# Performance work log

Hardware: AMD Instinct MI355X
Metric: run time of the kernel (lower is better)

## Reference

```python
import jax, jax.numpy as jnp
import numpy as np

N_NODES = 100000
N_EDGES = 800000
N_RADIAL = 16
H_NF = 64
VOCAB = 95  # Embedding(95, h_nf): atomic numbers


def swish(v):
    return v * jax.nn.sigmoid(v)


def setup_inputs() -> dict:
    key = jax.random.key(0)
    ks = jax.random.split(key, 10)
    coords = jax.random.randint(ks[0], (N_NODES,), 0, VOCAB)
    rbf = jax.random.normal(ks[1], (N_EDGES, N_RADIAL), dtype=jnp.float32)
    node_is = jax.random.randint(ks[2], (N_EDGES,), 0, N_NODES)
    node_js = jax.random.randint(ks[3], (N_EDGES,), 0, N_NODES)
    s = 0.05
    emb_W = jax.random.normal(ks[4], (VOCAB, H_NF), dtype=jnp.float32) * s
    W_rbf0 = jax.random.normal(ks[5], (N_RADIAL, H_NF), dtype=jnp.float32) * s
    b_rbf0 = jnp.zeros((H_NF,), dtype=jnp.float32)
    W_lin = jax.random.normal(ks[6], (3 * H_NF, H_NF), dtype=jnp.float32) * s
    b_lin = jnp.zeros((H_NF,), dtype=jnp.float32)
    W_rbf1 = jax.random.normal(ks[7], (N_RADIAL, H_NF), dtype=jnp.float32) * s  # no bias
    return {
        "coords": coords, "rbf": rbf, "node_is": node_is, "node_js": node_js,
        "emb_W": emb_W, "W_rbf0": W_rbf0, "b_rbf0": b_rbf0,
        "W_lin": W_lin, "b_lin": b_lin, "W_rbf1": W_rbf1,
    }


def reference(coords, rbf, node_is, node_js, emb_W, W_rbf0, b_rbf0, W_lin, b_lin, W_rbf1):
    # edge_model of FeatsInitLayer
    x = emb_W[coords]                              # [N, h] gather from embedding table
    rbf0 = swish(rbf @ W_rbf0 + b_rbf0)            # [E, h]
    cat = jnp.concatenate([x[node_is], x[node_js], rbf0], axis=-1)  # [E, 3h]
    e1 = swish(cat @ W_lin + b_lin)                # [E, h]
    e2 = (rbf @ W_rbf1) * e1                       # [E, h]
    return (e1, e2)
```

## Files before the change

### kernel.cpp

```cpp
#include <hip/hip_runtime.h>
#include <stdint.h>


#define N_NODES 100000
#define N_EDGES 800000
#define H_NF 64
#define VOCAB 95
#define NTILES (N_EDGES / 16)

typedef __attribute__((ext_vector_type(8))) short short8;
typedef __attribute__((ext_vector_type(4))) float f32x4;

#define TAB_STRIDE 66
#define TAB2_OFF   (VOCAB * TAB_STRIDE)
#define TAB_U16    (2 * VOCAB * TAB_STRIDE)
#define TAB_U16_PAD 12544
#define B0_OFF     TAB_U16_PAD
#define W3_OFF     (TAB_U16_PAD + 4096)

__device__ __forceinline__ unsigned short f2bf(float x) {
  uint32_t u = __float_as_uint(x);
  return (unsigned short)((u + 0x7FFFu + ((u >> 16) & 1u)) >> 16);
}
__device__ __forceinline__ float bf2f(unsigned short b) {
  return __uint_as_float(((uint32_t)b) << 16);
}
__device__ __forceinline__ float swish_f(float x) {
  return x * __builtin_amdgcn_rcpf(1.0f + __expf(-x));
}

__global__ void feats_prep(const float* __restrict__ emb_W,
                           const float* __restrict__ W_rbf0,
                           const float* __restrict__ b_rbf0,
                           const float* __restrict__ W_lin,
                           const float* __restrict__ b_lin,
                           const float* __restrict__ W_rbf1,
                           unsigned short* __restrict__ ws16) {
  const int b = blockIdx.x, t = threadIdx.x;
  if (b < VOCAB) {
    const int c = b, h = t;
    float e1 = 0.f, e2 = b_lin[h];
    for (int k = 0; k < 64; ++k) {
      const float w = emb_W[c * 64 + k];
      e1 += w * W_lin[k * 64 + h];
      e2 += w * W_lin[(64 + k) * 64 + h];
    }
    ws16[c * TAB_STRIDE + h] = f2bf(e1);
    ws16[TAB2_OFF + c * TAB_STRIDE + h] = f2bf(e2);
  } else if (b == VOCAB) {
    for (int idx = t; idx < 4096; idx += 64) {
      const int tt = idx >> 9, l = (idx >> 3) & 63, i = idx & 7;
      const int k = (l >> 4) * 8 + i, n = tt * 16 + (l & 15);
      float v = 0.f;
      if (k < 16)       v = (n < 64) ? W_rbf0[k * 64 + n] : W_rbf1[k * 64 + (n - 64)];
      else if (k == 16) v = (n < 64) ? b_rbf0[n] : 0.f;
      ws16[B0_OFF + idx] = f2bf(v);
    }
  } else {
    for (int idx = t; idx < 4096; idx += 64) {
      const int f = idx >> 9, l = (idx >> 3) & 63, i = idx & 7;
      const int s = f >> 2, tt = f & 3;
      const int k = s * 32 + (l >> 4) * 8 + i, n = tt * 16 + (l & 15);
      ws16[W3_OFF + idx] = f2bf(W_lin[(128 + k) * 64 + n]);
    }
  }
}

__global__ __launch_bounds__(256) void feats_main(
    const int* __restrict__ coords, const float* __restrict__ rbf,
    const int* __restrict__ node_is, const int* __restrict__ node_js,
    const unsigned short* __restrict__ ws16, float* __restrict__ out) {
  __shared__ __align__(16) unsigned short tab[TAB_U16_PAD];
  __shared__ __align__(16) unsigned short stage[4][16 * 72];

  const int tid = threadIdx.x;
  const int lane = tid & 63;
  const int wv = tid >> 6;
  const int g = lane >> 4;
  const int lm = lane & 15;

  {
    const uint32_t* src = (const uint32_t*)ws16;
    uint32_t* dst = (uint32_t*)tab;
    for (int i = tid; i < TAB_U16_PAD / 2; i += 256) dst[i] = src[i];
  }

  short8 b0f[8], w3f[2][4];
  {
    const short8* p = (const short8*)(ws16 + B0_OFF);
#pragma unroll
    for (int t = 0; t < 8; ++t) b0f[t] = p[t * 64 + lane];
    const short8* q = (const short8*)(ws16 + W3_OFF);
#pragma unroll
    for (int f = 0; f < 8; ++f) w3f[f >> 2][f & 3] = q[f * 64 + lane];
  }
  __syncthreads();

  float* out_e1 = out;
  float* out_e2 = out + (size_t)N_EDGES * H_NF;
  const f32x4 zf = {0.f, 0.f, 0.f, 0.f};
  unsigned short* st = &stage[wv][0];

  for (int tile = blockIdx.x * 4 + wv; tile < NTILES; tile += gridDim.x * 4) {
    const int ebase = tile << 4;
    const int e = ebase + lm;
    const int ci = coords[node_is[e]];
    const int cj = coords[node_js[e]];

    short8 af;
    if (lane < 32) {
      const float4* rp = (const float4*)(rbf + (size_t)e * 16 + g * 8);
      const float4 v0 = rp[0], v1 = rp[1];
      af[0] = f2bf(v0.x); af[1] = f2bf(v0.y); af[2] = f2bf(v0.z); af[3] = f2bf(v0.w);
      af[4] = f2bf(v1.x); af[5] = f2bf(v1.y); af[6] = f2bf(v1.z); af[7] = f2bf(v1.w);
    } else {
      af = (short8){0, 0, 0, 0, 0, 0, 0, 0};
      if (lane < 48) af[0] = (short)0x3F80;
    }

    f32x4 t0v[4], t1v[4];
#pragma unroll
    for (int t = 0; t < 4; ++t)
      t0v[t] = __builtin_amdgcn_mfma_f32_16x16x32_bf16(af, b0f[t], zf, 0, 0, 0);
#pragma unroll
    for (int t = 0; t < 4; ++t)
      t1v[t] = __builtin_amdgcn_mfma_f32_16x16x32_bf16(af, b0f[4 + t], zf, 0, 0, 0);

#pragma unroll
    for (int t = 0; t < 4; ++t)
#pragma unroll
      for (int q = 0; q < 4; ++q)
        st[(g * 4 + q) * 72 + t * 16 + lm] = f2bf(swish_f(t0v[t][q]));

    const short8 a2_0 = *(const short8*)&st[lm * 72 + g * 8];
    const short8 a2_1 = *(const short8*)&st[lm * 72 + 32 + g * 8];

    int cia[4], cja[4];
#pragma unroll
    for (int q = 0; q < 4; ++q) {
      cia[q] = __shfl(ci, g * 4 + q, 64);
      cja[q] = __shfl(cj, g * 4 + q, 64);
    }

#pragma unroll
    for (int t = 0; t < 4; ++t) {
      f32x4 acc = __builtin_amdgcn_mfma_f32_16x16x32_bf16(a2_0, w3f[0][t], zf, 0, 0, 0);
      acc = __builtin_amdgcn_mfma_f32_16x16x32_bf16(a2_1, w3f[1][t], acc, 0, 0, 0);
      const int hp = t * 16 + lm;
#pragma unroll
      for (int q = 0; q < 4; ++q) {
        const float x = acc[q]
                      + bf2f(tab[cia[q] * TAB_STRIDE + hp])
                      + bf2f(tab[TAB2_OFF + cja[q] * TAB_STRIDE + hp]);
        const float e1 = swish_f(x);
        const float e2 = t1v[t][q] * e1;
        const size_t o = (size_t)(ebase + g * 4 + q) * 64 + hp;
        out_e1[o] = e1;
        out_e2[o] = e2;
      }
    }
  }
}

extern "C" void kernel_launch(void* const* d_in, const int* in_sizes, int n_in,
                              void* d_out, int out_size, void* d_ws, size_t ws_size,
                              hipStream_t stream) {
  const int* coords    = (const int*)d_in[0];
  const float* rbf     = (const float*)d_in[1];
  const int* node_is   = (const int*)d_in[2];
  const int* node_js   = (const int*)d_in[3];
  const float* emb_W   = (const float*)d_in[4];
  const float* W_rbf0  = (const float*)d_in[5];
  const float* b_rbf0  = (const float*)d_in[6];
  const float* W_lin   = (const float*)d_in[7];
  const float* b_lin   = (const float*)d_in[8];
  const float* W_rbf1  = (const float*)d_in[9];
  unsigned short* ws16 = (unsigned short*)d_ws;
  float* out           = (float*)d_out;

  hipLaunchKernelGGL(feats_prep, dim3(VOCAB + 2), dim3(64), 0, stream,
                     emb_W, W_rbf0, b_rbf0, W_lin, b_lin, W_rbf1, ws16);
  hipLaunchKernelGGL(feats_main, dim3(1024), dim3(256), 0, stream,
                     coords, rbf, node_is, node_js, ws16, out);
}
```

Measured before the change: 547.9 us.

## Precompute packed edge coord ids, prefetch next tile, use nontemporal stores

Adds a separate gather kernel that resolves coords[node_is] and coords[node_js] per edge and packs both into one 16-bit id in workspace, so the main kernel no longer does dependent double gathers or shuffles. The main loop now software-prefetches the next tile's rbf and packed ids, moves the rbf1 MFMA into the output loop, widens the LDS table copy to 16-byte loads, and uses nontemporal loads and stores for streaming data. In exchange it adds an extra kernel launch and a round trip of the packed id array through memory.

```diff
diff --git a/kernel.cpp b/kernel.cpp
--- a/kernel.cpp
+++ b/kernel.cpp
@@ -10,13 +10,15 @@
 
 typedef __attribute__((ext_vector_type(8))) short short8;
 typedef __attribute__((ext_vector_type(4))) float f32x4;
+typedef __attribute__((ext_vector_type(4))) int i32x4;
+typedef __attribute__((ext_vector_type(4))) unsigned short u16x4;
 
 #define TAB_STRIDE 66
 #define TAB2_OFF   (VOCAB * TAB_STRIDE)
-#define TAB_U16    (2 * VOCAB * TAB_STRIDE)
 #define TAB_U16_PAD 12544
 #define B0_OFF     TAB_U16_PAD
 #define W3_OFF     (TAB_U16_PAD + 4096)
+#define CID_OFF    (TAB_U16_PAD + 8192)
 
 __device__ __forceinline__ unsigned short f2bf(float x) {
   uint32_t u = __float_as_uint(x);
@@ -66,10 +68,24 @@
   }
 }
 
+__global__ __launch_bounds__(256) void feats_gather(
+    const int* __restrict__ coords, const int* __restrict__ node_is,
+    const int* __restrict__ node_js, unsigned short* __restrict__ cid) {
+  const int idx = blockIdx.x * 256 + threadIdx.x;
+  if (idx >= N_EDGES / 4) return;
+  const i32x4 vi = __builtin_nontemporal_load((const i32x4*)node_is + idx);
+  const i32x4 vj = __builtin_nontemporal_load((const i32x4*)node_js + idx);
+  u16x4 r;
+  r.x = (unsigned short)(coords[vi.x] | (coords[vj.x] << 8));
+  r.y = (unsigned short)(coords[vi.y] | (coords[vj.y] << 8));
+  r.z = (unsigned short)(coords[vi.z] | (coords[vj.z] << 8));
+  r.w = (unsigned short)(coords[vi.w] | (coords[vj.w] << 8));
+  __builtin_nontemporal_store(r, (u16x4*)cid + idx);
+}
+
 __global__ __launch_bounds__(256) void feats_main(
-    const int* __restrict__ coords, const float* __restrict__ rbf,
-    const int* __restrict__ node_is, const int* __restrict__ node_js,
-    const unsigned short* __restrict__ ws16, float* __restrict__ out) {
+    const float* __restrict__ rbf, const unsigned short* __restrict__ ws16,
+    float* __restrict__ out) {
   __shared__ __align__(16) unsigned short tab[TAB_U16_PAD];
   __shared__ __align__(16) unsigned short stage[4][16 * 72];
 
@@ -78,11 +94,12 @@
   const int wv = tid >> 6;
   const int g = lane >> 4;
   const int lm = lane & 15;
+  const unsigned short* cid = ws16 + CID_OFF;
 
   {
-    const uint32_t* src = (const uint32_t*)ws16;
-    uint32_t* dst = (uint32_t*)tab;
-    for (int i = tid; i < TAB_U16_PAD / 2; i += 256) dst[i] = src[i];
+    const uint4* src = (const uint4*)ws16;
+    uint4* dst = (uint4*)tab;
+    for (int i = tid; i < TAB_U16_PAD / 8; i += 256) dst[i] = src[i];
   }
 
   short8 b0f[8], w3f[2][4];
@@ -100,31 +117,42 @@
   float* out_e2 = out + (size_t)N_EDGES * H_NF;
   const f32x4 zf = {0.f, 0.f, 0.f, 0.f};
   unsigned short* st = &stage[wv][0];
-
-  for (int tile = blockIdx.x * 4 + wv; tile < NTILES; tile += gridDim.x * 4) {
+  const int stride = gridDim.x * 4;
+
+  int tile = blockIdx.x * 4 + wv;
+
+  auto load_af = [&](int tl) -> short8 {
+    short8 a;
+    if (lane < 32) {
+      const f32x4* rp = (const f32x4*)(rbf + (size_t)(tl * 16 + lm) * 16 + g * 8);
+      const f32x4 v0 = __builtin_nontemporal_load(rp);
+      const f32x4 v1 = __builtin_nontemporal_load(rp + 1);
+      a[0] = f2bf(v0.x); a[1] = f2bf(v0.y); a[2] = f2bf(v0.z); a[3] = f2bf(v0.w);
+      a[4] = f2bf(v1.x); a[5] = f2bf(v1.y); a[6] = f2bf(v1.z); a[7] = f2bf(v1.w);
+    } else {
+      a = (short8){0, 0, 0, 0, 0, 0, 0, 0};
+      if (lane < 48) a[0] = (short)0x3F80;
+    }
+    return a;
+  };
+  auto load_cid = [&](int tl) -> u16x4 {
+    return *(const u16x4*)(cid + tl * 16 + g * 4);
+  };
+
+  short8 af = (tile < NTILES) ? load_af(tile) : short8{0,0,0,0,0,0,0,0};
+  u16x4 cv = (tile < NTILES) ? load_cid(tile) : u16x4{0,0,0,0};
+
+  for (; tile < NTILES; tile += stride) {
+    const int ntile = tile + stride;
+    short8 af_n = af; u16x4 cv_n = cv;
+    if (ntile < NTILES) { af_n = load_af(ntile); cv_n = load_cid(ntile); }
+
     const int ebase = tile << 4;
-    const int e = ebase + lm;
-    const int ci = coords[node_is[e]];
-    const int cj = coords[node_js[e]];
-
-    short8 af;
-    if (lane < 32) {
-      const float4* rp = (const float4*)(rbf + (size_t)e * 16 + g * 8);
-      const float4 v0 = rp[0], v1 = rp[1];
-      af[0] = f2bf(v0.x); af[1] = f2bf(v0.y); af[2] = f2bf(v0.z); af[3] = f2bf(v0.w);
-      af[4] = f2bf(v1.x); af[5] = f2bf(v1.y); af[6] = f2bf(v1.z); af[7] = f2bf(v1.w);
-    } else {
-      af = (short8){0, 0, 0, 0, 0, 0, 0, 0};
-      if (lane < 48) af[0] = (short)0x3F80;
-    }
-
-    f32x4 t0v[4], t1v[4];
+
+    f32x4 t0v[4];
 #pragma unroll
     for (int t = 0; t < 4; ++t)
       t0v[t] = __builtin_amdgcn_mfma_f32_16x16x32_bf16(af, b0f[t], zf, 0, 0, 0);
-#pragma unroll
-    for (int t = 0; t < 4; ++t)
-      t1v[t] = __builtin_amdgcn_mfma_f32_16x16x32_bf16(af, b0f[4 + t], zf, 0, 0, 0);
 
 #pragma unroll
     for (int t = 0; t < 4; ++t)
@@ -134,31 +162,28 @@
 
     const short8 a2_0 = *(const short8*)&st[lm * 72 + g * 8];
     const short8 a2_1 = *(const short8*)&st[lm * 72 + 32 + g * 8];
-
-    int cia[4], cja[4];
-#pragma unroll
-    for (int q = 0; q < 4; ++q) {
-      cia[q] = __shfl(ci, g * 4 + q, 64);
-      cja[q] = __shfl(cj, g * 4 + q, 64);
-    }
 
 #pragma unroll
     for (int t = 0; t < 4; ++t) {
       f32x4 acc = __builtin_amdgcn_mfma_f32_16x16x32_bf16(a2_0, w3f[0][t], zf, 0, 0, 0);
       acc = __builtin_amdgcn_mfma_f32_16x16x32_bf16(a2_1, w3f[1][t], acc, 0, 0, 0);
+      const f32x4 t1 = __builtin_amdgcn_mfma_f32_16x16x32_bf16(af, b0f[4 + t], zf, 0, 0, 0);
       const int hp = t * 16 + lm;
 #pragma unroll
       for (int q = 0; q < 4; ++q) {
+        const int ci = cv[q] & 0xFF, cj = cv[q] >> 8;
         const float x = acc[q]
-                      + bf2f(tab[cia[q] * TAB_STRIDE + hp])
-                      + bf2f(tab[TAB2_OFF + cja[q] * TAB_STRIDE + hp]);
+                      + bf2f(tab[ci * TAB_STRIDE + hp])
+                      + bf2f(tab[TAB2_OFF + cj * TAB_STRIDE + hp]);
         const float e1 = swish_f(x);
-        const float e2 = t1v[t][q] * e1;
+        const float e2 = t1[q] * e1;
         const size_t o = (size_t)(ebase + g * 4 + q) * 64 + hp;
-        out_e1[o] = e1;
-        out_e2[o] = e2;
+        __builtin_nontemporal_store(e1, &out_e1[o]);
+        __builtin_nontemporal_store(e2, &out_e2[o]);
       }
     }
+
+    af = af_n; cv = cv_n;
   }
 }
 
@@ -180,6 +205,8 @@
 
   hipLaunchKernelGGL(feats_prep, dim3(VOCAB + 2), dim3(64), 0, stream,
                      emb_W, W_rbf0, b_rbf0, W_lin, b_lin, W_rbf1, ws16);
+  hipLaunchKernelGGL(feats_gather, dim3((N_EDGES / 4 + 255) / 256), dim3(256), 0, stream,
+                     coords, node_is, node_js, ws16 + CID_OFF);
   hipLaunchKernelGGL(feats_main, dim3(1024), dim3(256), 0, stream,
-                     coords, rbf, node_is, node_js, ws16, out);
-}
+                     rbf, ws16, out);
+}
```

Measured after the change: 566.0 us. +3.3%, slower.
